# Optimization experiments

Hardware: AMD Instinct MI355X
Metric: run time of the kernel (lower is better)

Reference implementation:

```python
import jax, jax.numpy as jnp
import numpy as np

D_MODEL = 2048
N_HEADS = 16
HEAD_DIM = D_MODEL // N_HEADS
D_FF = 4 * D_MODEL


def setup_inputs() -> dict:
    key = jax.random.key(0)
    ks = jax.random.split(key, 12)
    s = 1.0 / np.sqrt(D_MODEL)
    sf = 1.0 / np.sqrt(D_FF)
    return {
        "x": jax.random.normal(ks[0], (2, 2048, D_MODEL), dtype=jnp.float32),
        "wq": jax.random.uniform(ks[1], (D_MODEL, D_MODEL), jnp.float32, -s, s),
        "wk": jax.random.uniform(ks[2], (D_MODEL, D_MODEL), jnp.float32, -s, s),
        "wv": jax.random.uniform(ks[3], (D_MODEL, D_MODEL), jnp.float32, -s, s),
        "wo": jax.random.uniform(ks[4], (D_MODEL, D_MODEL), jnp.float32, -s, s),
        "w1": jax.random.uniform(ks[5], (D_MODEL, D_FF), jnp.float32, -s, s),
        "b1": jax.random.uniform(ks[6], (D_FF,), jnp.float32, -s, s),
        "w2": jax.random.uniform(ks[7], (D_FF, D_MODEL), jnp.float32, -sf, sf),
        "b2": jax.random.uniform(ks[8], (D_MODEL,), jnp.float32, -sf, sf),
        "g1": jnp.ones((D_MODEL,), jnp.float32),
        "be1": jnp.zeros((D_MODEL,), jnp.float32),
        "g2": jnp.ones((D_MODEL,), jnp.float32),
        "be2": jnp.zeros((D_MODEL,), jnp.float32),
    }


def _layernorm(x, g, b, eps=1e-5):
    mu = jnp.mean(x, axis=-1, keepdims=True)
    var = jnp.mean(jnp.square(x - mu), axis=-1, keepdims=True)
    return (x - mu) * jax.lax.rsqrt(var + eps) * g + b


def reference(x, wq, wk, wv, wo, w1, b1, w2, b2, g1, be1, g2, be2):
    B, S, D = x.shape
    residual = x
    h = _layernorm(x, g1, be1)
    # [B,S,D] -> [B,H,S,hd]
    q = (h @ wq).reshape(B, S, N_HEADS, HEAD_DIM).transpose(0, 2, 1, 3)
    k = (h @ wk).reshape(B, S, N_HEADS, HEAD_DIM).transpose(0, 2, 1, 3)
    v = (h @ wv).reshape(B, S, N_HEADS, HEAD_DIM).transpose(0, 2, 1, 3)
    scores = jnp.einsum("bhqd,bhkd->bhqk", q, k) / np.sqrt(HEAD_DIM).astype(np.float32)
    attn = jax.nn.softmax(scores, axis=-1)
    out = jnp.einsum("bhqk,bhkd->bhqd", attn, v)
    out = out.transpose(0, 2, 1, 3).reshape(B, S, D) @ wo
    x = residual + out
    residual = x
    h = _layernorm(x, g2, be2)
    h = jax.nn.gelu(h @ w1 + b1, approximate=False) @ w2 + b2
    return residual + h
```

## Files before the change

### kernel.cpp

```cpp
#include <hip/hip_runtime.h>
#include <cstdint>
#include <cstddef>

#define DM   2048
#define NH   16
#define HD   128
#define DFF  8192
#define SEQ  2048
#define NB   2
#define NTOK (NB * SEQ)

using bf16x8 = __attribute__((ext_vector_type(8))) __bf16;
using f32x4  = __attribute__((ext_vector_type(4))) float;

__device__ __forceinline__ unsigned short f2bf(float f) {
  unsigned int u = __float_as_uint(f);
  u += 0x7fffu + ((u >> 16) & 1u);
  return (unsigned short)(u >> 16);
}

__device__ __forceinline__ void gload16(const void* g, void* l) {
  __builtin_amdgcn_global_load_lds(
      (const __attribute__((address_space(1))) unsigned int*)g,
      (__attribute__((address_space(3))) unsigned int*)l, 16, 0, 0);
}

__device__ __forceinline__ f32x4 mfma16(bf16x8 a, bf16x8 b, f32x4 c) {
  return __builtin_amdgcn_mfma_f32_16x16x32_bf16(a, b, c, 0, 0, 0);
}

#define BARRIER() asm volatile("s_barrier" ::: "memory")
#define LGKM0()   asm volatile("s_waitcnt lgkmcnt(0)" ::: "memory")

__device__ __forceinline__ int xcd_swz(int hb, int nwg) {
  return (hb & 7) * (nwg >> 3) + (hb >> 3);
}

__device__ __forceinline__ void tc64_body(
    const float* __restrict__ src, unsigned short* __restrict__ dst,
    int R, int C, int r0, int c0) {
  __shared__ float tile[64][65];
  const int t = threadIdx.x;
#pragma unroll
  for (int j = 0; j < 4; ++j) {
    const int c = t + j * 256;
    const int row = c >> 4, col = (c & 15) * 4;
    float4 v = *(const float4*)(src + (size_t)(r0 + row) * C + c0 + col);
    tile[row][col] = v.x; tile[row][col + 1] = v.y;
    tile[row][col + 2] = v.z; tile[row][col + 3] = v.w;
  }
  __syncthreads();
#pragma unroll
  for (int j = 0; j < 4; ++j) {
    const int c = t + j * 256;
    const int drow = c >> 4, scol = (c & 15) * 4;
    union { unsigned short u[4]; ushort4 v; } pk;
    pk.u[0] = f2bf(tile[scol][drow]);
    pk.u[1] = f2bf(tile[scol + 1][drow]);
    pk.u[2] = f2bf(tile[scol + 2][drow]);
    pk.u[3] = f2bf(tile[scol + 3][drow]);
    *(ushort4*)(dst + (size_t)(c0 + drow) * R + r0 + scol) = pk.v;
  }
}

__global__ __launch_bounds__(256) void transpose_cast(
    const float* __restrict__ src, unsigned short* __restrict__ dst, int R, int C) {
  tc64_body(src, dst, R, C, blockIdx.y * 64, blockIdx.x * 64);
}

__global__ __launch_bounds__(256) void transpose_cast4(
    const float* __restrict__ wq, const float* __restrict__ wk,
    const float* __restrict__ wv, const float* __restrict__ wo,
    unsigned short* __restrict__ dqkv, unsigned short* __restrict__ dwo) {
  const int z = blockIdx.z;
  const float* src = (z == 0) ? wq : (z == 1) ? wk : (z == 2) ? wv : wo;
  unsigned short* dst = (z < 3) ? (dqkv + (size_t)z * 2048 * 2048) : dwo;
  tc64_body(src, dst, 2048, 2048, blockIdx.y * 64, blockIdx.x * 64);
}

__global__ __launch_bounds__(256) void ln_kernel(
    const float* __restrict__ x, const float* __restrict__ gam,
    const float* __restrict__ bet, unsigned short* __restrict__ out) {
  const int row = blockIdx.x, tid = threadIdx.x;
  const float* xr = x + (size_t)row * DM;
  float4 a = *(const float4*)(xr + tid * 8);
  float4 b = *(const float4*)(xr + tid * 8 + 4);
  float s  = a.x + a.y + a.z + a.w + b.x + b.y + b.z + b.w;
  float s2 = a.x*a.x + a.y*a.y + a.z*a.z + a.w*a.w +
             b.x*b.x + b.y*b.y + b.z*b.z + b.w*b.w;
#pragma unroll
  for (int off = 32; off > 0; off >>= 1) {
    s  += __shfl_xor(s, off);
    s2 += __shfl_xor(s2, off);
  }
  __shared__ float red[8];
  const int wid = tid >> 6;
  if ((tid & 63) == 0) { red[wid] = s; red[4 + wid] = s2; }
  __syncthreads();
  s  = red[0] + red[1] + red[2] + red[3];
  s2 = red[4] + red[5] + red[6] + red[7];
  const float mean = s * (1.0f / DM);
  const float var  = s2 * (1.0f / DM) - mean * mean;
  const float rstd = rsqrtf(var + 1e-5f);
  float4 g0 = *(const float4*)(gam + tid * 8);
  float4 g1 = *(const float4*)(gam + tid * 8 + 4);
  float4 e0 = *(const float4*)(bet + tid * 8);
  float4 e1 = *(const float4*)(bet + tid * 8 + 4);
  union { unsigned short u[8]; uint4 v; } pk;
  const float* av = (const float*)&a; const float* bv = (const float*)&b;
  const float* gv0 = (const float*)&g0; const float* gv1 = (const float*)&g1;
  const float* ev0 = (const float*)&e0; const float* ev1 = (const float*)&e1;
#pragma unroll
  for (int j = 0; j < 4; j++) pk.u[j]     = f2bf((av[j] - mean) * rstd * gv0[j] + ev0[j]);
#pragma unroll
  for (int j = 0; j < 4; j++) pk.u[4 + j] = f2bf((bv[j] - mean) * rstd * gv1[j] + ev1[j]);
  *(uint4*)(out + (size_t)row * DM + tid * 8) = pk.v;
}

template <int EPI>
__global__ __launch_bounds__(512, 2) void gemm256(
    const unsigned short* __restrict__ A, const unsigned short* __restrict__ Bt,
    int M, int N, int K,
    unsigned short* __restrict__ o0, unsigned short* __restrict__ o1,
    unsigned short* __restrict__ o2, float* __restrict__ fo,
    const float* __restrict__ e0, const float* __restrict__ e1) {
  __shared__ __attribute__((aligned(16))) unsigned short As[2][256 * 64];
  __shared__ __attribute__((aligned(16))) unsigned short Bs[2][256 * 64];
  const int tid = threadIdx.x;
  const int wid = tid >> 6, lane = tid & 63;
  const int wr = wid >> 2, wc = wid & 3;
  const int c16 = lane & 15, g = lane >> 4;
  const int m0 = blockIdx.y * 256, n0 = blockIdx.x * 256;

  const int c0 = tid, c1 = tid + 512;
  const int r0_ = c0 >> 3, s0_ = ((c0 & 7) ^ (r0_ & 7)) * 8;
  const int r1_ = c1 >> 3, s1_ = ((c1 & 7) ^ (r1_ & 7)) * 8;
  const unsigned short* a0p = A + (size_t)(m0 + r0_) * K + s0_;
  const unsigned short* a1p = A + (size_t)(m0 + r1_) * K + s1_;
  const unsigned short* b0p = Bt + (size_t)(n0 + r0_) * K + s0_;
  const unsigned short* b1p = Bt + (size_t)(n0 + r1_) * K + s1_;
  const size_t hstep = (size_t)128 * K;

  auto SA = [&](int buf, int h, int kt) {
    gload16(a0p + h * hstep + kt * 64, &As[buf][h * 8192 + c0 * 8]);
    gload16(a1p + h * hstep + kt * 64, &As[buf][h * 8192 + c1 * 8]);
  };
  auto SB = [&](int buf, int h, int kt) {
    gload16(b0p + h * hstep + kt * 64, &Bs[buf][h * 8192 + c0 * 8]);
    gload16(b1p + h * hstep + kt * 64, &Bs[buf][h * 8192 + c1 * 8]);
  };

  const int swz   = (c16 & 7) << 4;
  const int k0off = (g * 16) ^ swz;
  const int k1off = (64 + g * 16) ^ swz;

  f32x4 acc[8][4];
#pragma unroll
  for (int i = 0; i < 8; i++)
#pragma unroll
    for (int j = 0; j < 4; j++) acc[i][j] = f32x4{0.f, 0.f, 0.f, 0.f};

  bf16x8 af0[4][2], af1[4][2], bf0[2][2], bf1[2][2];

  const int NT = K >> 6;
  SA(0, 0, 0); SA(0, 1, 0); SB(0, 0, 0); SB(0, 1, 0);
  SB(1, 0, 1); SB(1, 1, 1); SA(1, 0, 1);
  asm volatile("s_waitcnt vmcnt(6)" ::: "memory");
  BARRIER();

  for (int t = 0; t < NT; ++t) {
    const int buf = t & 1;
    const char* Ac = (const char*)As[buf];
    const char* Bc = (const char*)Bs[buf];
    const bool st = (t + 2) < NT;
#pragma unroll
    for (int mi = 0; mi < 4; ++mi) {
      const int rb = (wr * 64 + mi * 16 + c16) * 128;
      af0[mi][0] = *(const bf16x8*)(Ac + rb + k0off);
      af0[mi][1] = *(const bf16x8*)(Ac + rb + k1off);
    }
#pragma unroll
    for (int ni = 0; ni < 2; ++ni) {
      const int rb = (wc * 32 + ni * 16 + c16) * 128;
      bf0[ni][0] = *(const bf16x8*)(Bc + rb + k0off);
      bf0[ni][1] = *(const bf16x8*)(Bc + rb + k1off);
    }
    if (t + 1 < NT) SA(buf ^ 1, 1, t + 1);
    BARRIER(); LGKM0();
    __builtin_amdgcn_s_setprio(1);
#pragma unroll
    for (int mi = 0; mi < 4; ++mi)
#pragma unroll
      for (int ni = 0; ni < 2; ++ni)
#pragma unroll
        for (int kk = 0; kk < 2; ++kk)
          acc[mi][ni] = mfma16(af0[mi][kk], bf0[ni][kk], acc[mi][ni]);
    __builtin_amdgcn_s_setprio(0);
    BARRIER();
#pragma unroll
    for (int ni = 0; ni < 2; ++ni) {
      const int rb = (128 + wc * 32 + ni * 16 + c16) * 128;
      bf1[ni][0] = *(const bf16x8*)(Bc + rb + k0off);
      bf1[ni][1] = *(const bf16x8*)(Bc + rb + k1off);
    }
    if (st) SB(buf, 0, t + 2);
    BARRIER(); LGKM0();
    __builtin_amdgcn_s_setprio(1);
#pragma unroll
    for (int mi = 0; mi < 4; ++mi)
#pragma unroll
      for (int ni = 0; ni < 2; ++ni)
#pragma unroll
        for (int kk = 0; kk < 2; ++kk)
          acc[mi][2 + ni] = mfma16(af0[mi][kk], bf1[ni][kk], acc[mi][2 + ni]);
    __builtin_amdgcn_s_setprio(0);
    BARRIER();
#pragma unroll
    for (int mi = 0; mi < 4; ++mi) {
      const int rb = (128 + wr * 64 + mi * 16 + c16) * 128;
      af1[mi][0] = *(const bf16x8*)(Ac + rb + k0off);
      af1[mi][1] = *(const bf16x8*)(Ac + rb + k1off);
    }
    if (st) SB(buf, 1, t + 2);
    BARRIER(); LGKM0();
    __builtin_amdgcn_s_setprio(1);
#pragma unroll
    for (int mi = 0; mi < 4; ++mi)
#pragma unroll
      for (int ni = 0; ni < 2; ++ni)
#pragma unroll
        for (int kk = 0; kk < 2; ++kk)
          acc[4 + mi][2 + ni] = mfma16(af1[mi][kk], bf1[ni][kk], acc[4 + mi][2 + ni]);
    __builtin_amdgcn_s_setprio(0);
    BARRIER();
    if (st) SA(buf, 0, t + 2);
    BARRIER();
    __builtin_amdgcn_s_setprio(1);
#pragma unroll
    for (int mi = 0; mi < 4; ++mi)
#pragma unroll
      for (int ni = 0; ni < 2; ++ni)
#pragma unroll
        for (int kk = 0; kk < 2; ++kk)
          acc[4 + mi][ni] = mfma16(af1[mi][kk], bf0[ni][kk], acc[4 + mi][ni]);
    __builtin_amdgcn_s_setprio(0);
    if (st) { asm volatile("s_waitcnt vmcnt(6)" ::: "memory"); }
    else    { asm volatile("s_waitcnt vmcnt(0)" ::: "memory"); }
    BARRIER();
  }

#pragma unroll
  for (int mi = 0; mi < 8; ++mi) {
    const int arow = (mi < 4) ? (wr * 64 + mi * 16) : (128 + wr * 64 + (mi - 4) * 16);
#pragma unroll
    for (int ni = 0; ni < 4; ++ni) {
      const int bcol = (ni < 2) ? (wc * 32 + ni * 16) : (128 + wc * 32 + (ni - 2) * 16);
#pragma unroll
      for (int r = 0; r < 4; ++r) {
        const int row = m0 + arow + g * 4 + r;
        const int col = n0 + bcol + c16;
        const float v = acc[mi][ni][r];
        if constexpr (EPI == 2) {
          const float t2 = v + e0[col];
          const float ge = 0.5f * t2 * (1.0f + erff(t2 * 0.7071067811865476f));
          o0[(size_t)row * N + col] = f2bf(ge);
        } else {
          const size_t idx = (size_t)row * N + col;
          fo[idx] = (EPI == 1) ? (e0[idx] + v) : (e1[idx] + v + e0[col]);
        }
      }
    }
  }
}

template <int EPI>
__global__ __launch_bounds__(256, 2) void gemm128(
    const unsigned short* __restrict__ A, const unsigned short* __restrict__ Bt,
    int M, int N, int K,
    unsigned short* __restrict__ o0, unsigned short* __restrict__ o1,
    unsigned short* __restrict__ o2, float* __restrict__ fo,
    const float* __restrict__ e0, const float* __restrict__ e1) {
  __shared__ __attribute__((aligned(16))) unsigned short SM[4][128 * 64];
  const int tid = threadIdx.x;
  const int wid = tid >> 6, lane = tid & 63;
  const int m0 = blockIdx.y * 128, n0 = blockIdx.x * 128;
  const int wr = wid >> 1, wc = wid & 1;
  const int c16 = lane & 15, g = lane >> 4;

  const unsigned short *ap[4], *bp[4];
  int dsto[4];
#pragma unroll
  for (int j = 0; j < 4; ++j) {
    const int c = tid + j * 256;
    const int r = c >> 3, s = ((c & 7) ^ (r & 7)) * 8;
    ap[j] = A + (size_t)(m0 + r) * K + s;
    bp[j] = Bt + (size_t)(n0 + r) * K + s;
    dsto[j] = c * 8;
  }
  auto SA = [&](int buf, int kt) {
#pragma unroll
    for (int j = 0; j < 4; ++j) gload16(ap[j] + kt * 64, &SM[buf][dsto[j]]);
  };
  auto SB = [&](int buf, int kt) {
#pragma unroll
    for (int j = 0; j < 4; ++j) gload16(bp[j] + kt * 64, &SM[2 + buf][dsto[j]]);
  };

  const int swz   = (c16 & 7) << 4;
  const int k0off = (g * 16) ^ swz;
  const int k1off = (64 + g * 16) ^ swz;

  f32x4 acc[4][4];
#pragma unroll
  for (int i = 0; i < 4; i++)
#pragma unroll
    for (int j = 0; j < 4; j++) acc[i][j] = f32x4{0.f, 0.f, 0.f, 0.f};

  bf16x8 af[4][2], bfm[4][2];

  const int NT = K >> 6;
  SA(0, 0); SB(0, 0);
  __syncthreads();

  for (int t = 0; t < NT; ++t) {
    const int buf = t & 1;
    const char* Ac = (const char*)SM[buf];
    const char* Bc = (const char*)SM[2 + buf];
    if (t + 1 < NT) { SA(buf ^ 1, t + 1); SB(buf ^ 1, t + 1); }
#pragma unroll
    for (int mi = 0; mi < 4; ++mi) {
      const int rb = (wr * 64 + mi * 16 + c16) * 128;
      af[mi][0] = *(const bf16x8*)(Ac + rb + k0off);
      af[mi][1] = *(const bf16x8*)(Ac + rb + k1off);
    }
#pragma unroll
    for (int ni = 0; ni < 4; ++ni) {
      const int rb = (wc * 64 + ni * 16 + c16) * 128;
      bfm[ni][0] = *(const bf16x8*)(Bc + rb + k0off);
      bfm[ni][1] = *(const bf16x8*)(Bc + rb + k1off);
    }
    __builtin_amdgcn_s_setprio(1);
#pragma unroll
    for (int mi = 0; mi < 4; ++mi)
#pragma unroll
      for (int ni = 0; ni < 4; ++ni)
#pragma unroll
        for (int kk = 0; kk < 2; ++kk)
          acc[mi][ni] = mfma16(af[mi][kk], bfm[ni][kk], acc[mi][ni]);
    __builtin_amdgcn_s_setprio(0);
    __syncthreads();
  }

  if constexpr (EPI == 0) {
    const int which = n0 >> 11;
    if (which == 2) {
      unsigned short* Ls = &SM[0][0];
#pragma unroll
      for (int mi = 0; mi < 4; ++mi)
#pragma unroll
        for (int ni = 0; ni < 4; ++ni)
#pragma unroll
          for (int r = 0; r < 4; ++r) {
            const int s_loc = wr * 64 + mi * 16 + g * 4 + r;
            const int d_loc = wc * 64 + ni * 16 + c16;
            Ls[d_loc * 136 + s_loc] = f2bf(acc[mi][ni][r]);
          }
      __syncthreads();
      const int b  = m0 >> 11, s0v = m0 & 2047;
      const int hh = (n0 & 2047) >> 7;
      const size_t base = (size_t)(b * NH + hh) * HD * (size_t)SEQ;
#pragma unroll
      for (int it2 = 0; it2 < 2; ++it2) {
        const int hd = it2 * 64 + (tid >> 2);
        const int sc = (tid & 3) * 32;
#pragma unroll
        for (int j = 0; j < 4; ++j) {
          uint4 vv = *(const uint4*)&Ls[hd * 136 + sc + j * 8];
          *(uint4*)&o2[base + (size_t)hd * SEQ + s0v + sc + j * 8] = vv;
        }
      }
    } else {
#pragma unroll
      for (int mi = 0; mi < 4; ++mi)
#pragma unroll
        for (int ni = 0; ni < 4; ++ni)
#pragma unroll
          for (int r = 0; r < 4; ++r) {
            const int row = m0 + wr * 64 + mi * 16 + g * 4 + r;
            const int col = n0 + wc * 64 + ni * 16 + c16;
            const float v = acc[mi][ni][r];
            const int b = row >> 11, s = row & 2047;
            const int d = col & 2047;
            const int hh = d >> 7, hd = d & 127;
            const size_t bh = (size_t)(b * NH + hh);
            if (which == 0) o0[(bh * SEQ + s) * HD + hd] = f2bf(v * 0.127517434f);
            else            o1[(bh * SEQ + s) * HD + hd] = f2bf(v);
          }
    }
  } else {
#pragma unroll
    for (int mi = 0; mi < 4; ++mi) {
#pragma unroll
      for (int ni = 0; ni < 4; ++ni) {
#pragma unroll
        for (int r = 0; r < 4; ++r) {
          const int row = m0 + wr * 64 + mi * 16 + g * 4 + r;
          const int col = n0 + wc * 64 + ni * 16 + c16;
          const float v = acc[mi][ni][r];
          if constexpr (EPI == 2) {
            const float t2 = v + e0[col];
            const float ge = 0.5f * t2 * (1.0f + erff(t2 * 0.7071067811865476f));
            o0[(size_t)row * N + col] = f2bf(ge);
          } else {
            const size_t idx = (size_t)row * N + col;
            fo[idx] = (EPI == 1) ? (e0[idx] + v) : (e1[idx] + v + e0[col]);
          }
        }
      }
    }
  }
}

__global__ __launch_bounds__(256, 2) void attn_kernel(
    const unsigned short* __restrict__ q, const unsigned short* __restrict__ k,
    const unsigned short* __restrict__ vT, unsigned short* __restrict__ out) {
  __shared__ __attribute__((aligned(16))) unsigned short Ks[2][64 * 128];
  __shared__ __attribute__((aligned(16))) unsigned short Vs[2][128 * 64];
  __shared__ __attribute__((aligned(16))) unsigned short Ps[4 * 32 * 64];
  const int tid = threadIdx.x, wid = tid >> 6, lane = tid & 63;
  const int c16 = lane & 15, g = lane >> 4;
  const int vbk = xcd_swz(blockIdx.x, 512);
  const int qt = vbk & 15, h = (vbk >> 4) & 15, b = vbk >> 8;
  const int q0 = qt * 128;
  const unsigned short* qb = q + (size_t)(b * NH + h) * SEQ * HD;
  const unsigned short* kb = k + (size_t)(b * NH + h) * SEQ * HD;
  const unsigned short* vb = vT + (size_t)(b * NH + h) * HD * SEQ;

  bf16x8 aq[2][4];
#pragma unroll
  for (int mi = 0; mi < 2; mi++)
#pragma unroll
    for (int ks = 0; ks < 4; ks++)
      aq[mi][ks] = *(const bf16x8*)(qb + (size_t)(q0 + wid * 32 + mi * 16 + c16) * HD +
                                    ks * 32 + g * 8);

  f32x4 o[2][8] = {};
  float mrow[2][4], lrow[2][4];
#pragma unroll
  for (int mi = 0; mi < 2; mi++)
#pragma unroll
    for (int r = 0; r < 4; r++) { mrow[mi][r] = -1e30f; lrow[mi][r] = 0.f; }

  const int kRowB = tid >> 4;
  const int kChk  = (tid & 15) ^ (kRowB & 7);
  const int vRowB = tid >> 3;
  const int vChk  = (tid & 7) ^ (vRowB & 7);
  char* PsW = (char*)Ps + wid * 4096;

  auto STAGE = [&](int buf, int kv0) {
#pragma unroll
    for (int seg = 0; seg < 4; seg++) {
      gload16(kb + (size_t)(kv0 + seg * 16 + kRowB) * HD + kChk * 8,
              &Ks[buf][wid * 512 + seg * 2048]);
      gload16(vb + (size_t)(seg * 32 + vRowB) * SEQ + kv0 + vChk * 8,
              &Vs[buf][wid * 512 + seg * 2048]);
    }
  };

  STAGE(0, 0);
  __syncthreads();

  const int NIT = SEQ / 64;
  for (int it = 0; it < NIT; ++it) {
    const int cur = it & 1;
    if (it + 1 < NIT) STAGE(cur ^ 1, (it + 1) * 64);
    const char* Kc = (const char*)&Ks[cur][0];
    const char* Vc = (const char*)&Vs[cur][0];

    f32x4 sc[2][4] = {};
#pragma unroll
    for (int ks = 0; ks < 4; ks++) {
#pragma unroll
      for (int ni = 0; ni < 4; ni++) {
        const int kr = ni * 16 + c16;
        const int lin = kr * 256 + ks * 64 + g * 16;
        bf16x8 bk = *(const bf16x8*)(Kc + (lin ^ ((kr & 7) << 4)));
        sc[0][ni] = mfma16(aq[0][ks], bk, sc[0][ni]);
        sc[1][ni] = mfma16(aq[1][ks], bk, sc[1][ni]);
      }
    }

#pragma unroll
    for (int mi = 0; mi < 2; mi++) {
#pragma unroll
      for (int r = 0; r < 4; r++) {
        float pm = fmaxf(fmaxf(sc[mi][0][r], sc[mi][1][r]),
                         fmaxf(sc[mi][2][r], sc[mi][3][r]));
        pm = fmaxf(pm, __shfl_xor(pm, 1));
        pm = fmaxf(pm, __shfl_xor(pm, 2));
        pm = fmaxf(pm, __shfl_xor(pm, 4));
        pm = fmaxf(pm, __shfl_xor(pm, 8));
        if (!__all(pm <= mrow[mi][r])) {
          const float mnew = fmaxf(mrow[mi][r], pm);
          const float scal = exp2f(mrow[mi][r] - mnew);
          mrow[mi][r] = mnew;
          lrow[mi][r] *= scal;
#pragma unroll
          for (int nj = 0; nj < 8; nj++) o[mi][nj][r] *= scal;
        }
        float rs = 0.f;
        const int prow = mi * 16 + g * 4 + r;
#pragma unroll
        for (int ni = 0; ni < 4; ni++) {
          const float p = exp2f(sc[mi][ni][r] - mrow[mi][r]);
          rs += p;
          const int lin = prow * 128 + (ni * 16 + c16) * 2;
          *(unsigned short*)(PsW + (lin ^ ((prow & 7) << 4))) = f2bf(p);
        }
        lrow[mi][r] += rs;
      }
    }

#pragma unroll
    for (int ks2 = 0; ks2 < 2; ks2++) {
      bf16x8 pa[2];
#pragma unroll
      for (int mi = 0; mi < 2; mi++) {
        const int pr = mi * 16 + c16;
        const int lin = pr * 128 + ks2 * 64 + g * 16;
        pa[mi] = *(const bf16x8*)(PsW + (lin ^ ((pr & 7) << 4)));
      }
#pragma unroll
      for (int nj = 0; nj < 8; nj++) {
        const int vr = nj * 16 + c16;
        const int lin = vr * 128 + ks2 * 64 + g * 16;
        bf16x8 bv = *(const bf16x8*)(Vc + (lin ^ ((vr & 7) << 4)));
        o[0][nj] = mfma16(pa[0], bv, o[0][nj]);
        o[1][nj] = mfma16(pa[1], bv, o[1][nj]);
      }
    }
    __syncthreads();
  }

#pragma unroll
  for (int mi = 0; mi < 2; mi++)
#pragma unroll
    for (int r = 0; r < 4; r++) {
      float l = lrow[mi][r];
      l += __shfl_xor(l, 1);
      l += __shfl_xor(l, 2);
      l += __shfl_xor(l, 4);
      l += __shfl_xor(l, 8);
      const float inv = 1.0f / l;
      const int s = q0 + wid * 32 + mi * 16 + g * 4 + r;
#pragma unroll
      for (int nj = 0; nj < 8; nj++)
        out[((size_t)(b * SEQ + s)) * DM + h * HD + nj * 16 + c16] =
            f2bf(o[mi][nj][r] * inv);
    }
}

extern "C" void kernel_launch(void* const* d_in, const int* in_sizes, int n_in,
                              void* d_out, int out_size, void* d_ws, size_t ws_size,
                              hipStream_t stream) {
  const float* x  = (const float*)d_in[0];
  const float* wq = (const float*)d_in[1];
  const float* wk = (const float*)d_in[2];
  const float* wv = (const float*)d_in[3];
  const float* wo = (const float*)d_in[4];
  const float* w1 = (const float*)d_in[5];
  const float* b1 = (const float*)d_in[6];
  const float* w2 = (const float*)d_in[7];
  const float* b2 = (const float*)d_in[8];
  const float* g1 = (const float*)d_in[9];
  const float* be1 = (const float*)d_in[10];
  const float* g2 = (const float*)d_in[11];
  const float* be2 = (const float*)d_in[12];

  char* ws = (char*)d_ws;
  unsigned short* wqkvT = (unsigned short*)(ws + 0);
  unsigned short* woT   = (unsigned short*)(ws + 25165824);
  unsigned short* w1T   = (unsigned short*)(ws + 33554432);
  unsigned short* w2T   = (unsigned short*)(ws + 67108864);
  float*          x2    = (float*)(ws + 100663296);
  unsigned short* hbuf  = (unsigned short*)(ws + 134217728);
  unsigned short* qbuf  = (unsigned short*)(ws + 150994944);
  unsigned short* kbuf  = (unsigned short*)(ws + 167772160);
  unsigned short* vtbuf = (unsigned short*)(ws + 184549376);
  unsigned short* ffh   = (unsigned short*)(ws + 150994944);

  transpose_cast4<<<dim3(32, 32, 4), 256, 0, stream>>>(wq, wk, wv, wo, wqkvT, woT);
  transpose_cast<<<dim3(128, 32), 256, 0, stream>>>(w1, w1T, 2048, 8192);
  transpose_cast<<<dim3(32, 128), 256, 0, stream>>>(w2, w2T, 8192, 2048);

  ln_kernel<<<NTOK, 256, 0, stream>>>(x, g1, be1, hbuf);

  gemm128<0><<<dim3(48, 32), 256, 0, stream>>>(
      hbuf, wqkvT, NTOK, 6144, 2048, qbuf, kbuf, vtbuf, nullptr, nullptr, nullptr);

  attn_kernel<<<512, 256, 0, stream>>>(qbuf, kbuf, vtbuf, hbuf);

  gemm128<1><<<dim3(16, 32), 256, 0, stream>>>(
      hbuf, woT, NTOK, 2048, 2048, nullptr, nullptr, nullptr, x2, x, nullptr);

  ln_kernel<<<NTOK, 256, 0, stream>>>(x2, g2, be2, hbuf);

  gemm256<2><<<dim3(32, 16), 512, 0, stream>>>(
      hbuf, w1T, NTOK, DFF, 2048, ffh, nullptr, nullptr, nullptr, b1, nullptr);

  gemm128<3><<<dim3(16, 32), 256, 0, stream>>>(
      ffh, w2T, NTOK, 2048, DFF, nullptr, nullptr, nullptr, (float*)d_out, b2, x2);
}
```

Before: 633.8 us.

## Collapse GEMM main loop from four LDS phases to two with batched prefetch

Restructures the per-k-tile schedule of the bf16 GEMM: both B fragment halves are read from LDS up front, and the MFMA work runs in two larger phases instead of four. The prefetch issues for the next-next tile (SB halves and SA half 0) are now grouped together before the second phase. This removes two barrier pairs per iteration and lengthens uninterrupted MFMA runs. In exchange it raises register pressure and reduces how finely global-to-LDS loads interleave with compute. It also risks LDS hazards if a buffer is overwritten while other waves may still be reading it.

```diff
diff --git a/kernel.cpp b/kernel.cpp
--- a/kernel.cpp
+++ b/kernel.cpp
@@ -181,9 +181,12 @@
     }
 #pragma unroll
     for (int ni = 0; ni < 2; ++ni) {
-      const int rb = (wc * 32 + ni * 16 + c16) * 128;
-      bf0[ni][0] = *(const bf16x8*)(Bc + rb + k0off);
-      bf0[ni][1] = *(const bf16x8*)(Bc + rb + k1off);
+      const int rb0 = (wc * 32 + ni * 16 + c16) * 128;
+      bf0[ni][0] = *(const bf16x8*)(Bc + rb0 + k0off);
+      bf0[ni][1] = *(const bf16x8*)(Bc + rb0 + k1off);
+      const int rb1 = (128 + wc * 32 + ni * 16 + c16) * 128;
+      bf1[ni][0] = *(const bf16x8*)(Bc + rb1 + k0off);
+      bf1[ni][1] = *(const bf16x8*)(Bc + rb1 + k1off);
     }
     if (t + 1 < NT) SA(buf ^ 1, 1, t + 1);
     BARRIER(); LGKM0();
@@ -193,26 +196,10 @@
 #pragma unroll
       for (int ni = 0; ni < 2; ++ni)
 #pragma unroll
-        for (int kk = 0; kk < 2; ++kk)
-          acc[mi][ni] = mfma16(af0[mi][kk], bf0[ni][kk], acc[mi][ni]);
-    __builtin_amdgcn_s_setprio(0);
-    BARRIER();
-#pragma unroll
-    for (int ni = 0; ni < 2; ++ni) {
-      const int rb = (128 + wc * 32 + ni * 16 + c16) * 128;
-      bf1[ni][0] = *(const bf16x8*)(Bc + rb + k0off);
-      bf1[ni][1] = *(const bf16x8*)(Bc + rb + k1off);
-    }
-    if (st) SB(buf, 0, t + 2);
-    BARRIER(); LGKM0();
-    __builtin_amdgcn_s_setprio(1);
-#pragma unroll
-    for (int mi = 0; mi < 4; ++mi)
-#pragma unroll
-      for (int ni = 0; ni < 2; ++ni)
-#pragma unroll
-        for (int kk = 0; kk < 2; ++kk)
+        for (int kk = 0; kk < 2; ++kk) {
+          acc[mi][ni]     = mfma16(af0[mi][kk], bf0[ni][kk], acc[mi][ni]);
           acc[mi][2 + ni] = mfma16(af0[mi][kk], bf1[ni][kk], acc[mi][2 + ni]);
+        }
     __builtin_amdgcn_s_setprio(0);
     BARRIER();
 #pragma unroll
@@ -221,7 +208,7 @@
       af1[mi][0] = *(const bf16x8*)(Ac + rb + k0off);
       af1[mi][1] = *(const bf16x8*)(Ac + rb + k1off);
     }
-    if (st) SB(buf, 1, t + 2);
+    if (st) { SB(buf, 0, t + 2); SB(buf, 1, t + 2); SA(buf, 0, t + 2); }
     BARRIER(); LGKM0();
     __builtin_amdgcn_s_setprio(1);
 #pragma unroll
@@ -229,20 +216,10 @@
 #pragma unroll
       for (int ni = 0; ni < 2; ++ni)
 #pragma unroll
-        for (int kk = 0; kk < 2; ++kk)
+        for (int kk = 0; kk < 2; ++kk) {
           acc[4 + mi][2 + ni] = mfma16(af1[mi][kk], bf1[ni][kk], acc[4 + mi][2 + ni]);
-    __builtin_amdgcn_s_setprio(0);
-    BARRIER();
-    if (st) SA(buf, 0, t + 2);
-    BARRIER();
-    __builtin_amdgcn_s_setprio(1);
-#pragma unroll
-    for (int mi = 0; mi < 4; ++mi)
-#pragma unroll
-      for (int ni = 0; ni < 2; ++ni)
-#pragma unroll
-        for (int kk = 0; kk < 2; ++kk)
-          acc[4 + mi][ni] = mfma16(af1[mi][kk], bf0[ni][kk], acc[4 + mi][ni]);
+          acc[4 + mi][ni]     = mfma16(af1[mi][kk], bf0[ni][kk], acc[4 + mi][ni]);
+        }
     __builtin_amdgcn_s_setprio(0);
     if (st) { asm volatile("s_waitcnt vmcnt(6)" ::: "memory"); }
     else    { asm volatile("s_waitcnt vmcnt(0)" ::: "memory"); }
```

Result: no change. 633.2 us (-0.1%).
